# Kernel optimization log

Measured on AMD Instinct MI355X. Metric: run time of the kernel, lower is better.

The kernel has to match this reference:

```python
import jax, jax.numpy as jnp
import numpy as np

EMBED_DIM = 1024
NUM_HEADS = 16
HEAD_DIM = EMBED_DIM // NUM_HEADS
SCALING = HEAD_DIM ** -0.5
TGT_LEN, BSZ = 2048, 2


def setup_inputs() -> dict:
    key = jax.random.key(0)
    k1, k2, k3 = jax.random.split(key, 3)
    return {
        "query": jax.random.normal(k1, (TGT_LEN, BSZ, EMBED_DIM), jnp.float32),
        "in_proj_weight": jax.random.normal(k2, (3 * EMBED_DIM, EMBED_DIM), jnp.float32) * (EMBED_DIM ** -0.5),
        "in_proj_bias": jnp.zeros((3 * EMBED_DIM,), jnp.float32),
        "out_w": jax.random.normal(k3, (EMBED_DIM, EMBED_DIM), jnp.float32) * (EMBED_DIM ** -0.5),
        "out_b": jnp.zeros((EMBED_DIM,), jnp.float32),
    }


def reference(query, in_proj_weight, in_proj_bias, out_w, out_b):
    tgt_len, bsz, embed_dim = query.shape
    # fused QKV projection (self-attention path: qkv_same)
    qkv = query @ in_proj_weight.T + in_proj_bias  # [T, B, 3E]
    q, k, v = jnp.split(qkv, 3, axis=-1)
    q = q * SCALING
    # [T, B, E] -> [B*H, T, hd]
    def to_heads(x):
        return x.reshape(tgt_len, bsz * NUM_HEADS, HEAD_DIM).transpose(1, 0, 2)
    q, k, v = to_heads(q), to_heads(k), to_heads(v)
    attn_weights = jnp.einsum('bqd,bkd->bqk', q, k)          # [B*H, T, T]
    attn_weights = jax.nn.softmax(attn_weights, axis=-1)
    attn = jnp.einsum('bqk,bkd->bqd', attn_weights, v)       # [B*H, T, hd]
    attn = attn.transpose(1, 0, 2).reshape(tgt_len, bsz, embed_dim)
    attn = attn @ out_w.T + out_b
    # averaged attention weights over heads (need_weights=True)
    avg_weights = attn_weights.reshape(bsz, NUM_HEADS, tgt_len, tgt_len).mean(axis=1)
    return attn, avg_weights
```

## Files before the change

kernel.cpp:

```cpp
#include <hip/hip_runtime.h>
#include <hip/hip_bf16.h>
#include <math.h>

#define T_LEN 2048
#define BSZ   2
#define EMB   1024
#define NH    16
#define HD    64
#define BHN   (BSZ*NH)
#define M1    (T_LEN*BSZ)
#define SCAL  0.125f
#define QSCALE (0.125f * 1.44269504088896f)

typedef __attribute__((ext_vector_type(8))) short bf16x8;
typedef __attribute__((ext_vector_type(4))) float f32x4;
typedef __attribute__((ext_vector_type(2))) unsigned int u32x2;

__device__ inline unsigned short f2bf(float x) {
    union { float f; unsigned u; } v; v.f = x;
    unsigned r = v.u + 0x7FFF + ((v.u >> 16) & 1);
    return (unsigned short)(r >> 16);
}

__device__ inline unsigned pack2bf(float a, float b) {
    union { __hip_bfloat162 h; unsigned u; } v;
    v.h = __float22bfloat162_rn(make_float2(a, b));
    return v.u;
}

__device__ inline float fexp2(float x) {
#if __has_builtin(__builtin_amdgcn_exp2f)
    return __builtin_amdgcn_exp2f(x);
#else
    return exp2f(x);
#endif
}

__device__ inline void async16(const unsigned short* g, unsigned short* l) {
    __builtin_amdgcn_global_load_lds(
        (const __attribute__((address_space(1))) void*)g,
        (__attribute__((address_space(3))) void*)l, 16, 0, 0);
}

__device__ inline void hard_barrier() {
    __builtin_amdgcn_sched_barrier(0);
    asm volatile("" ::: "memory");
    __builtin_amdgcn_s_barrier();
    asm volatile("" ::: "memory");
    __builtin_amdgcn_sched_barrier(0);
}

__device__ inline unsigned short* swz(unsigned short* base, int r, int c) {
    return base + (((r << 3) + (c ^ (r & 7))) << 3);
}
__device__ inline const unsigned short* swz(const unsigned short* base, int r, int c) {
    return base + (((r << 3) + (c ^ (r & 7))) << 3);
}

__device__ inline void xchg(unsigned e, unsigned o, unsigned& w_lo, unsigned& w_hi) {
#if __has_builtin(__builtin_amdgcn_permlane32_swap) && __has_builtin(__builtin_amdgcn_permlane16_swap)
    u32x2 x = __builtin_amdgcn_permlane32_swap(e, o, false, false);
    u32x2 y = __builtin_amdgcn_permlane16_swap(x[0], x[1], false, false);
    w_lo = y[0]; w_hi = y[1];
#else
    int lane = (int)(threadIdx.x & 63);
    int quad = lane >> 4, l16 = lane & 15;
    int srcA = ((quad & 1) * 2) * 16 + l16;
    int srcB = ((quad & 1) * 2 + 1) * 16 + l16;
    unsigned ea = (unsigned)__shfl((int)e, srcA, 64);
    unsigned oa = (unsigned)__shfl((int)o, srcA, 64);
    unsigned eb = (unsigned)__shfl((int)e, srcB, 64);
    unsigned ob = (unsigned)__shfl((int)o, srcB, 64);
    w_lo = (quad >> 1) ? oa : ea;
    w_hi = (quad >> 1) ? ob : eb;
#endif
}

__global__ __launch_bounds__(256) void cvt3_kernel(
    const float* __restrict__ s0, const float* __restrict__ s1,
    const float* __restrict__ s2, unsigned short* __restrict__ dst,
    int n0, int n1)
{
    int idx = blockIdx.x * 256 + threadIdx.x;
    const float* src; int o;
    if (idx < n0)           { src = s0; o = idx; }
    else if (idx < n0 + n1) { src = s1; o = idx - n0; }
    else                    { src = s2; o = idx - n0 - n1; }
    float4 a = reinterpret_cast<const float4*>(src)[(size_t)o * 2];
    float4 c = reinterpret_cast<const float4*>(src)[(size_t)o * 2 + 1];
    unsigned w[4] = { pack2bf(a.x, a.y), pack2bf(a.z, a.w),
                      pack2bf(c.x, c.y), pack2bf(c.z, c.w) };
    reinterpret_cast<uint4*>(dst)[idx] = *reinterpret_cast<uint4*>(w);
}

__global__ __launch_bounds__(256) void qkv_mfma_kernel(
    const unsigned short* __restrict__ A, const unsigned short* __restrict__ B,
    const float* __restrict__ bias,
    unsigned short* __restrict__ Q16, unsigned short* __restrict__ K16,
    unsigned short* __restrict__ Vt16)
{
    constexpr int BM = 128, BN = 128, BK = 32, K = 1024;
    __shared__ unsigned short As[BM * BK];
    __shared__ unsigned short Bs[BN * BK];
    const int tid = threadIdx.x;
    const int lane = tid & 63, wave = tid >> 6;
    const int quad = lane >> 4, l16 = lane & 15;
    const int wr = wave >> 1, wc = wave & 1;
    const int m0 = blockIdx.x * BM, n0 = blockIdx.y * BN;

    f32x4 zero4 = {0.f, 0.f, 0.f, 0.f};
    f32x4 acc[4][4];
    #pragma unroll
    for (int i = 0; i < 4; ++i)
        #pragma unroll
        for (int j = 0; j < 4; ++j) acc[i][j] = zero4;

    for (int k0 = 0; k0 < K; k0 += BK) {
        __syncthreads();
        #pragma unroll
        for (int t = 0; t < 2; ++t) {
            int c = t * 256 + tid;
            int m = c >> 2, kb = c & 3;
            async16(&A[(size_t)(m0 + m) * K + k0 + kb * 8], &As[c * 8]);
            async16(&B[(size_t)(n0 + m) * K + k0 + kb * 8], &Bs[c * 8]);
        }
        __syncthreads();
        bf16x8 af[4], bfr[4];
        #pragma unroll
        for (int i = 0; i < 4; ++i) {
            af[i]  = *reinterpret_cast<const bf16x8*>(&As[(wr * 64 + i * 16 + l16) * BK + quad * 8]);
            bfr[i] = *reinterpret_cast<const bf16x8*>(&Bs[(wc * 64 + i * 16 + l16) * BK + quad * 8]);
        }
        #pragma unroll
        for (int i = 0; i < 4; ++i)
            #pragma unroll
            for (int j = 0; j < 4; ++j)
                acc[i][j] = __builtin_amdgcn_mfma_f32_16x16x32_bf16(af[i], bfr[j], acc[i][j], 0, 0, 0);
    }

    #pragma unroll
    for (int j = 0; j < 4; ++j) {
        int n = n0 + wc * 64 + j * 16 + l16;
        float bv = bias[n];
        int which = n >> 10;
        int c = n & 1023;
        int h = c >> 6, d = c & 63;
        #pragma unroll
        for (int i = 0; i < 4; ++i) {
            #pragma unroll
            for (int r = 0; r < 4; ++r) {
                int m = m0 + wr * 64 + i * 16 + quad * 4 + r;
                int t = m >> 1, b = m & 1;
                int bh = b * NH + h;
                float v = acc[i][j][r] + bv;
                if (which == 0)      Q16[((size_t)bh * T_LEN + t) * HD + d] = f2bf(v * QSCALE);
                else if (which == 1) K16[((size_t)bh * T_LEN + t) * HD + d] = f2bf(v);
                else                 Vt16[((size_t)bh * HD + d) * T_LEN + t] = f2bf(v);
            }
        }
    }
}

__global__ __launch_bounds__(256) void flash_mfma_kernel(
    const unsigned short* __restrict__ Qb, const unsigned short* __restrict__ Kb,
    const unsigned short* __restrict__ Vt, unsigned short* __restrict__ AO,
    float* __restrict__ Rrow)
{
    __shared__ unsigned short Ks[2][64 * 64];
    __shared__ unsigned short Vs[2][64 * 64];
    const int tid = threadIdx.x;
    const int lane = tid & 63, wave = tid >> 6;
    const int quad = lane >> 4, l16 = lane & 15;

    const int lin = blockIdx.y * gridDim.x + blockIdx.x;
    const int xcd = lin & 7, slot = lin >> 3;
    const int bh = xcd * 4 + (slot >> 5);
    const int qt = slot & 31;
    const int q0 = qt * 64;
    const int b = bh >> 4, h = bh & 15;

    const unsigned short* Qp = Qb + ((size_t)bh * T_LEN + q0 + wave * 16 + l16) * HD;
    bf16x8 qf0 = *reinterpret_cast<const bf16x8*>(Qp + quad * 8);
    bf16x8 qf1 = *reinterpret_cast<const bf16x8*>(Qp + 32 + quad * 8);

    f32x4 zero4 = {0.f, 0.f, 0.f, 0.f};
    f32x4 oacc[4] = {zero4, zero4, zero4, zero4};
    float l_i = 0.f;

    const unsigned short* Kbase = Kb + (size_t)bh * T_LEN * HD;
    const unsigned short* Vbase = Vt + (size_t)bh * HD * T_LEN;

    const int cl0 = tid, cl1 = tid + 256;
    const int r0 = cl0 >> 3, c0 = (cl0 & 7) ^ (r0 & 7);
    const int r1 = cl1 >> 3, c1 = (cl1 & 7) ^ (r1 & 7);

    async16(&Kbase[(size_t)r0 * HD + c0 * 8], &Ks[0][cl0 * 8]);
    async16(&Kbase[(size_t)r1 * HD + c1 * 8], &Ks[0][cl1 * 8]);
    async16(&Vbase[(size_t)r0 * T_LEN + c0 * 8], &Vs[0][cl0 * 8]);
    async16(&Vbase[(size_t)r1 * T_LEN + c1 * 8], &Vs[0][cl1 * 8]);

    int cur = 0;
    for (int kt = 0; kt < T_LEN; kt += 64) {
        if (kt + 64 < T_LEN) {
            const int nb = cur ^ 1, nkt = kt + 64;
            async16(&Kbase[(size_t)(nkt + r0) * HD + c0 * 8], &Ks[nb][cl0 * 8]);
            async16(&Kbase[(size_t)(nkt + r1) * HD + c1 * 8], &Ks[nb][cl1 * 8]);
            async16(&Vbase[(size_t)r0 * T_LEN + nkt + c0 * 8], &Vs[nb][cl0 * 8]);
            async16(&Vbase[(size_t)r1 * T_LEN + nkt + c1 * 8], &Vs[nb][cl1 * 8]);
            asm volatile("s_waitcnt vmcnt(4)" ::: "memory");
        } else {
            asm volatile("s_waitcnt vmcnt(0)" ::: "memory");
        }
        hard_barrier();

        const unsigned short* Kt = Ks[cur];
        const unsigned short* Vv = Vs[cur];

        f32x4 sacc[4] = {zero4, zero4, zero4, zero4};
        __builtin_amdgcn_s_setprio(1);
        #pragma unroll
        for (int kb = 0; kb < 4; ++kb) {
            bf16x8 kf0 = *reinterpret_cast<const bf16x8*>(swz(Kt, kb * 16 + l16, quad));
            sacc[kb] = __builtin_amdgcn_mfma_f32_16x16x32_bf16(kf0, qf0, sacc[kb], 0, 0, 0);
            bf16x8 kf1 = *reinterpret_cast<const bf16x8*>(swz(Kt, kb * 16 + l16, 4 + quad));
            sacc[kb] = __builtin_amdgcn_mfma_f32_16x16x32_bf16(kf1, qf1, sacc[kb], 0, 0, 0);
        }
        __builtin_amdgcn_s_setprio(0);

        float psum = 0.f;
        unsigned dlo[4], dhi[4];
        #pragma unroll
        for (int kb = 0; kb < 4; ++kb) {
            float p0 = fexp2(sacc[kb][0]);
            float p1 = fexp2(sacc[kb][1]);
            float p2 = fexp2(sacc[kb][2]);
            float p3 = fexp2(sacc[kb][3]);
            psum += (p0 + p1) + (p2 + p3);
            dlo[kb] = pack2bf(p0, p1);
            dhi[kb] = pack2bf(p2, p3);
        }
        psum += __shfl_xor(psum, 16);
        psum += __shfl_xor(psum, 32);
        l_i += psum;

        bf16x8 pfrag[2];
        #pragma unroll
        for (int s = 0; s < 2; ++s) {
            unsigned w0, w1, w2, w3;
            xchg(dlo[2 * s], dlo[2 * s + 1], w0, w2);
            xchg(dhi[2 * s], dhi[2 * s + 1], w1, w3);
            union { bf16x8 v; unsigned u[4]; } P;
            P.u[0] = w0; P.u[1] = w1; P.u[2] = w2; P.u[3] = w3;
            pfrag[s] = P.v;
        }

        __builtin_amdgcn_s_setprio(1);
        #pragma unroll
        for (int s = 0; s < 2; ++s) {
            #pragma unroll
            for (int dt = 0; dt < 4; ++dt) {
                bf16x8 va = *reinterpret_cast<const bf16x8*>(swz(Vv, dt * 16 + l16, s * 4 + quad));
                oacc[dt] = __builtin_amdgcn_mfma_f32_16x16x32_bf16(va, pfrag[s], oacc[dt], 0, 0, 0);
            }
        }
        __builtin_amdgcn_s_setprio(0);

        hard_barrier();
        cur ^= 1;
    }

    float rl = 1.0f / l_i;
    int q = q0 + wave * 16 + l16;
    size_t base = ((size_t)q * BSZ + b) * EMB + h * HD;
    #pragma unroll
    for (int dt = 0; dt < 4; ++dt) {
        unsigned o[2] = { pack2bf(oacc[dt][0] * rl, oacc[dt][1] * rl),
                          pack2bf(oacc[dt][2] * rl, oacc[dt][3] * rl) };
        *reinterpret_cast<uint2*>(&AO[base + dt * 16 + quad * 4]) = *reinterpret_cast<uint2*>(o);
    }
    if (quad == 0)
        Rrow[(size_t)bh * T_LEN + q] = rl;
}

__global__ __launch_bounds__(256) void avg_mfma_kernel(
    const unsigned short* __restrict__ Qb, const unsigned short* __restrict__ Kb,
    const float* __restrict__ Rrow, float* __restrict__ avg_out)
{
    __shared__ unsigned short Ks[2][2][64 * 64];
    const int tid = threadIdx.x;
    const int lane = tid & 63, wave = tid >> 6;
    const int quad = lane >> 4, l16 = lane & 15;
    const int kt = blockIdx.x, qt = blockIdx.y, b = blockIdx.z;
    const int q0 = qt * 128, k0 = kt * 64;

    auto stage_pair = [&](int buf, int h0) {
        const unsigned short* Kg = Kb + ((size_t)(b * NH + h0) * T_LEN + k0) * HD;
        #pragma unroll
        for (int t = 0; t < 4; ++t) {
            int c = t * 256 + tid;
            int hh = c >> 9, cl = c & 511;
            int r = cl >> 3, cc = (cl & 7) ^ (r & 7);
            async16(&Kg[(size_t)hh * T_LEN * HD + (size_t)r * HD + cc * 8],
                    &Ks[buf][0][0] + (size_t)c * 8);
        }
    };

    f32x4 zero4 = {0.f, 0.f, 0.f, 0.f};
    f32x4 acc[2][4];
    #pragma unroll
    for (int s = 0; s < 2; ++s)
        #pragma unroll
        for (int c = 0; c < 4; ++c) acc[s][c] = zero4;

    stage_pair(0, 0);
    int cur = 0;
    for (int g = 0; g < NH / 2; ++g) {
        if (g + 1 < NH / 2) {
            stage_pair(cur ^ 1, 2 * (g + 1));
            asm volatile("s_waitcnt vmcnt(4)" ::: "memory");
        } else {
            asm volatile("s_waitcnt vmcnt(0)" ::: "memory");
        }
        hard_barrier();

        #pragma unroll
        for (int hh = 0; hh < 2; ++hh) {
            const int bh = b * NH + 2 * g + hh;
            const unsigned short* Kt = Ks[cur][hh];
            bf16x8 kf[4][2];
            #pragma unroll
            for (int c = 0; c < 4; ++c) {
                kf[c][0] = *reinterpret_cast<const bf16x8*>(swz(Kt, c * 16 + l16, quad));
                kf[c][1] = *reinterpret_cast<const bf16x8*>(swz(Kt, c * 16 + l16, 4 + quad));
            }
            #pragma unroll
            for (int s = 0; s < 2; ++s) {
                const int qrow = q0 + s * 64 + wave * 16;
                const unsigned short* Qp = Qb + ((size_t)bh * T_LEN + qrow + l16) * HD;
                bf16x8 qf0 = *reinterpret_cast<const bf16x8*>(Qp + quad * 8);
                bf16x8 qf1 = *reinterpret_cast<const bf16x8*>(Qp + 32 + quad * 8);
                float4 rlv = *reinterpret_cast<const float4*>(
                    &Rrow[(size_t)bh * T_LEN + qrow + quad * 4]);

                f32x4 sacc[4] = {zero4, zero4, zero4, zero4};
                __builtin_amdgcn_s_setprio(1);
                #pragma unroll
                for (int c = 0; c < 4; ++c) {
                    sacc[c] = __builtin_amdgcn_mfma_f32_16x16x32_bf16(qf0, kf[c][0], sacc[c], 0, 0, 0);
                    sacc[c] = __builtin_amdgcn_mfma_f32_16x16x32_bf16(qf1, kf[c][1], sacc[c], 0, 0, 0);
                }
                __builtin_amdgcn_s_setprio(0);

                float rl4[4] = { rlv.x, rlv.y, rlv.z, rlv.w };
                #pragma unroll
                for (int c = 0; c < 4; ++c)
                    #pragma unroll
                    for (int r = 0; r < 4; ++r)
                        acc[s][c][r] += fexp2(sacc[c][r]) * rl4[r];
            }
        }
        hard_barrier();
        cur ^= 1;
    }

    #pragma unroll
    for (int s = 0; s < 2; ++s)
        #pragma unroll
        for (int r = 0; r < 4; ++r) {
            int q = q0 + s * 64 + wave * 16 + quad * 4 + r;
            size_t base = ((size_t)b * T_LEN + q) * T_LEN + k0;
            #pragma unroll
            for (int c = 0; c < 4; ++c)
                avg_out[base + c * 16 + l16] = acc[s][c][r] * (1.0f / 16.0f);
        }
}

__global__ __launch_bounds__(256) void out_mfma_kernel(
    const unsigned short* __restrict__ A, const unsigned short* __restrict__ B,
    const float* __restrict__ bias, float* __restrict__ out)
{
    constexpr int BM = 128, BN = 128, BK = 32, K = 1024;
    __shared__ unsigned short As[BM * BK];
    __shared__ unsigned short Bs[BN * BK];
    const int tid = threadIdx.x;
    const int lane = tid & 63, wave = tid >> 6;
    const int quad = lane >> 4, l16 = lane & 15;
    const int wr = wave >> 1, wc = wave & 1;
    const int m0 = blockIdx.x * BM, n0 = blockIdx.y * BN;

    f32x4 zero4 = {0.f, 0.f, 0.f, 0.f};
    f32x4 acc[4][4];
    #pragma unroll
    for (int i = 0; i < 4; ++i)
        #pragma unroll
        for (int j = 0; j < 4; ++j) acc[i][j] = zero4;

    for (int k0 = 0; k0 < K; k0 += BK) {
        __syncthreads();
        #pragma unroll
        for (int t = 0; t < 2; ++t) {
            int c = t * 256 + tid;
            int m = c >> 2, kb = c & 3;
            async16(&A[(size_t)(m0 + m) * K + k0 + kb * 8], &As[c * 8]);
            async16(&B[(size_t)(n0 + m) * K + k0 + kb * 8], &Bs[c * 8]);
        }
        __syncthreads();
        bf16x8 af[4], bfr[4];
        #pragma unroll
        for (int i = 0; i < 4; ++i) {
            af[i]  = *reinterpret_cast<const bf16x8*>(&As[(wr * 64 + i * 16 + l16) * BK + quad * 8]);
            bfr[i] = *reinterpret_cast<const bf16x8*>(&Bs[(wc * 64 + i * 16 + l16) * BK + quad * 8]);
        }
        #pragma unroll
        for (int i = 0; i < 4; ++i)
            #pragma unroll
            for (int j = 0; j < 4; ++j)
                acc[i][j] = __builtin_amdgcn_mfma_f32_16x16x32_bf16(af[i], bfr[j], acc[i][j], 0, 0, 0);
    }

    #pragma unroll
    for (int j = 0; j < 4; ++j) {
        int n = n0 + wc * 64 + j * 16 + l16;
        float bv = bias[n];
        #pragma unroll
        for (int i = 0; i < 4; ++i) {
            #pragma unroll
            for (int r = 0; r < 4; ++r) {
                int m = m0 + wr * 64 + i * 16 + quad * 4 + r;
                out[(size_t)m * 1024 + n] = acc[i][j][r] + bv;
            }
        }
    }
}

extern "C" void kernel_launch(void* const* d_in, const int* in_sizes, int n_in,
                              void* d_out, int out_size, void* d_ws, size_t ws_size,
                              hipStream_t stream)
{
    const float* query = (const float*)d_in[0];
    const float* wqkv  = (const float*)d_in[1];
    const float* bqkv  = (const float*)d_in[2];
    const float* wout  = (const float*)d_in[3];
    const float* bout  = (const float*)d_in[4];
    float* out = (float*)d_out;

    char* ws = (char*)d_ws;
    const size_t E_Q   = (size_t)M1 * EMB;
    const size_t E_W   = (size_t)3 * EMB * EMB;
    const size_t E_WO  = (size_t)EMB * EMB;
    const size_t E_QKV = (size_t)BHN * T_LEN * HD;

    unsigned short* queryb = (unsigned short*)ws;
    unsigned short* wqkvb  = queryb + E_Q;
    unsigned short* woutb  = wqkvb + E_W;
    unsigned short* Q16    = woutb + E_WO;
    unsigned short* K16    = Q16 + E_QKV;
    unsigned short* Vt16   = K16 + E_QKV;
    unsigned short* AO16   = Vt16 + E_QKV;
    float* Lr = (float*)(AO16 + E_Q);
    const size_t need = (E_Q + E_W + E_WO + 4 * E_QKV) * 2 + (size_t)BHN * T_LEN * 4;
    if (ws_size < need) return;

    cvt3_kernel<<<(int)((E_Q + E_W + E_WO) / 8 / 256), 256, 0, stream>>>(
        query, wqkv, wout, queryb, (int)(E_Q / 8), (int)(E_W / 8));

    qkv_mfma_kernel<<<dim3(M1 / 128, 3072 / 128), 256, 0, stream>>>(queryb, wqkvb, bqkv, Q16, K16, Vt16);
    flash_mfma_kernel<<<dim3(T_LEN / 64, BHN), 256, 0, stream>>>(Q16, K16, Vt16, AO16, Lr);
    avg_mfma_kernel<<<dim3(T_LEN / 64, T_LEN / 128, BSZ), 256, 0, stream>>>(Q16, K16, Lr, out + (size_t)M1 * EMB);
    out_mfma_kernel<<<dim3(M1 / 128, 1024 / 128), 256, 0, stream>>>(AO16, woutb, bout, out);
}
```

Measured before the change: 252.2 us.

## Double flash attention query tile per block and relax barrier scheduling fences

Each wave in the flash kernel now handles two 16-row query slices, so a block covers 128 queries. K fragments are loaded once and reused across both slices, and each V fragment feeds two MFMAs. This halves the K/V tile loads per query and the grid size (512 blocks instead of 1024). The sched_barrier fences around s_barrier are removed in both attention kernels so the compiler can schedule across barriers, and launch bounds request 2 blocks per EU. The costs are higher register pressure and fewer blocks to fill the GPU.

```diff
diff --git a/kernel.cpp b/kernel.cpp
--- a/kernel.cpp
+++ b/kernel.cpp
@@ -42,12 +42,10 @@
         (__attribute__((address_space(3))) void*)l, 16, 0, 0);
 }
 
-__device__ inline void hard_barrier() {
-    __builtin_amdgcn_sched_barrier(0);
+__device__ inline void bar() {
     asm volatile("" ::: "memory");
     __builtin_amdgcn_s_barrier();
     asm volatile("" ::: "memory");
-    __builtin_amdgcn_sched_barrier(0);
 }
 
 __device__ inline unsigned short* swz(unsigned short* base, int r, int c) {
@@ -161,7 +159,7 @@
     }
 }
 
-__global__ __launch_bounds__(256) void flash_mfma_kernel(
+__global__ __launch_bounds__(256, 2) void flash_mfma_kernel(
     const unsigned short* __restrict__ Qb, const unsigned short* __restrict__ Kb,
     const unsigned short* __restrict__ Vt, unsigned short* __restrict__ AO,
     float* __restrict__ Rrow)
@@ -174,18 +172,27 @@
 
     const int lin = blockIdx.y * gridDim.x + blockIdx.x;
     const int xcd = lin & 7, slot = lin >> 3;
-    const int bh = xcd * 4 + (slot >> 5);
-    const int qt = slot & 31;
-    const int q0 = qt * 64;
+    const int bh = xcd * 4 + (slot >> 4);
+    const int qt = slot & 15;
+    const int q0 = qt * 128;
     const int b = bh >> 4, h = bh & 15;
 
-    const unsigned short* Qp = Qb + ((size_t)bh * T_LEN + q0 + wave * 16 + l16) * HD;
-    bf16x8 qf0 = *reinterpret_cast<const bf16x8*>(Qp + quad * 8);
-    bf16x8 qf1 = *reinterpret_cast<const bf16x8*>(Qp + 32 + quad * 8);
+    bf16x8 qf[2][2];
+    #pragma unroll
+    for (int s = 0; s < 2; ++s) {
+        const unsigned short* Qp =
+            Qb + ((size_t)bh * T_LEN + q0 + wave * 32 + s * 16 + l16) * HD;
+        qf[s][0] = *reinterpret_cast<const bf16x8*>(Qp + quad * 8);
+        qf[s][1] = *reinterpret_cast<const bf16x8*>(Qp + 32 + quad * 8);
+    }
 
     f32x4 zero4 = {0.f, 0.f, 0.f, 0.f};
-    f32x4 oacc[4] = {zero4, zero4, zero4, zero4};
-    float l_i = 0.f;
+    f32x4 oacc[2][4];
+    #pragma unroll
+    for (int s = 0; s < 2; ++s)
+        #pragma unroll
+        for (int dt = 0; dt < 4; ++dt) oacc[s][dt] = zero4;
+    float l_i[2] = {0.f, 0.f};
 
     const unsigned short* Kbase = Kb + (size_t)bh * T_LEN * HD;
     const unsigned short* Vbase = Vt + (size_t)bh * HD * T_LEN;
@@ -211,75 +218,87 @@
         } else {
             asm volatile("s_waitcnt vmcnt(0)" ::: "memory");
         }
-        hard_barrier();
+        bar();
 
         const unsigned short* Kt = Ks[cur];
         const unsigned short* Vv = Vs[cur];
 
-        f32x4 sacc[4] = {zero4, zero4, zero4, zero4};
+        bf16x8 kf[4][2];
+        #pragma unroll
+        for (int kb = 0; kb < 4; ++kb) {
+            kf[kb][0] = *reinterpret_cast<const bf16x8*>(swz(Kt, kb * 16 + l16, quad));
+            kf[kb][1] = *reinterpret_cast<const bf16x8*>(swz(Kt, kb * 16 + l16, 4 + quad));
+        }
+
+        bf16x8 pfrag[2][2];
+        #pragma unroll
+        for (int s = 0; s < 2; ++s) {
+            f32x4 sacc[4] = {zero4, zero4, zero4, zero4};
+            __builtin_amdgcn_s_setprio(1);
+            #pragma unroll
+            for (int kb = 0; kb < 4; ++kb) {
+                sacc[kb] = __builtin_amdgcn_mfma_f32_16x16x32_bf16(kf[kb][0], qf[s][0], sacc[kb], 0, 0, 0);
+                sacc[kb] = __builtin_amdgcn_mfma_f32_16x16x32_bf16(kf[kb][1], qf[s][1], sacc[kb], 0, 0, 0);
+            }
+            __builtin_amdgcn_s_setprio(0);
+
+            float psum = 0.f;
+            unsigned dlo[4], dhi[4];
+            #pragma unroll
+            for (int kb = 0; kb < 4; ++kb) {
+                float p0 = fexp2(sacc[kb][0]);
+                float p1 = fexp2(sacc[kb][1]);
+                float p2 = fexp2(sacc[kb][2]);
+                float p3 = fexp2(sacc[kb][3]);
+                psum += (p0 + p1) + (p2 + p3);
+                dlo[kb] = pack2bf(p0, p1);
+                dhi[kb] = pack2bf(p2, p3);
+            }
+            psum += __shfl_xor(psum, 16);
+            psum += __shfl_xor(psum, 32);
+            l_i[s] += psum;
+
+            #pragma unroll
+            for (int s2 = 0; s2 < 2; ++s2) {
+                unsigned w0, w1, w2, w3;
+                xchg(dlo[2 * s2], dlo[2 * s2 + 1], w0, w2);
+                xchg(dhi[2 * s2], dhi[2 * s2 + 1], w1, w3);
+                union { bf16x8 v; unsigned u[4]; } P;
+                P.u[0] = w0; P.u[1] = w1; P.u[2] = w2; P.u[3] = w3;
+                pfrag[s][s2] = P.v;
+            }
+        }
+
         __builtin_amdgcn_s_setprio(1);
         #pragma unroll
-        for (int kb = 0; kb < 4; ++kb) {
-            bf16x8 kf0 = *reinterpret_cast<const bf16x8*>(swz(Kt, kb * 16 + l16, quad));
-            sacc[kb] = __builtin_amdgcn_mfma_f32_16x16x32_bf16(kf0, qf0, sacc[kb], 0, 0, 0);
-            bf16x8 kf1 = *reinterpret_cast<const bf16x8*>(swz(Kt, kb * 16 + l16, 4 + quad));
-            sacc[kb] = __builtin_amdgcn_mfma_f32_16x16x32_bf16(kf1, qf1, sacc[kb], 0, 0, 0);
+        for (int ks = 0; ks < 2; ++ks) {
+            #pragma unroll
+            for (int dt = 0; dt < 4; ++dt) {
+                bf16x8 va = *reinterpret_cast<const bf16x8*>(swz(Vv, dt * 16 + l16, ks * 4 + quad));
+                oacc[0][dt] = __builtin_amdgcn_mfma_f32_16x16x32_bf16(va, pfrag[0][ks], oacc[0][dt], 0, 0, 0);
+                oacc[1][dt] = __builtin_amdgcn_mfma_f32_16x16x32_bf16(va, pfrag[1][ks], oacc[1][dt], 0, 0, 0);
+            }
         }
         __builtin_amdgcn_s_setprio(0);
 
-        float psum = 0.f;
-        unsigned dlo[4], dhi[4];
-        #pragma unroll
-        for (int kb = 0; kb < 4; ++kb) {
-            float p0 = fexp2(sacc[kb][0]);
-            float p1 = fexp2(sacc[kb][1]);
-            float p2 = fexp2(sacc[kb][2]);
-            float p3 = fexp2(sacc[kb][3]);
-            psum += (p0 + p1) + (p2 + p3);
-            dlo[kb] = pack2bf(p0, p1);
-            dhi[kb] = pack2bf(p2, p3);
-        }
-        psum += __shfl_xor(psum, 16);
-        psum += __shfl_xor(psum, 32);
-        l_i += psum;
-
-        bf16x8 pfrag[2];
-        #pragma unroll
-        for (int s = 0; s < 2; ++s) {
-            unsigned w0, w1, w2, w3;
-            xchg(dlo[2 * s], dlo[2 * s + 1], w0, w2);
-            xchg(dhi[2 * s], dhi[2 * s + 1], w1, w3);
-            union { bf16x8 v; unsigned u[4]; } P;
-            P.u[0] = w0; P.u[1] = w1; P.u[2] = w2; P.u[3] = w3;
-            pfrag[s] = P.v;
-        }
-
-        __builtin_amdgcn_s_setprio(1);
-        #pragma unroll
-        for (int s = 0; s < 2; ++s) {
-            #pragma unroll
-            for (int dt = 0; dt < 4; ++dt) {
-                bf16x8 va = *reinterpret_cast<const bf16x8*>(swz(Vv, dt * 16 + l16, s * 4 + quad));
-                oacc[dt] = __builtin_amdgcn_mfma_f32_16x16x32_bf16(va, pfrag[s], oacc[dt], 0, 0, 0);
-            }
-        }
-        __builtin_amdgcn_s_setprio(0);
-
-        hard_barrier();
+        bar();
         cur ^= 1;
     }
 
-    float rl = 1.0f / l_i;
-    int q = q0 + wave * 16 + l16;
-    size_t base = ((size_t)q * BSZ + b) * EMB + h * HD;
-    #pragma unroll
-    for (int dt = 0; dt < 4; ++dt) {
-        unsigned o[2] = { pack2bf(oacc[dt][0] * rl, oacc[dt][1] * rl),
-                          pack2bf(oacc[dt][2] * rl, oacc[dt][3] * rl) };
-        *reinterpret_cast<uint2*>(&AO[base + dt * 16 + quad * 4]) = *reinterpret_cast<uint2*>(o);
-    }
-    if (quad == 0)
-        Rrow[(size_t)bh * T_LEN + q] = rl;
+    #pragma unroll
+    for (int s = 0; s < 2; ++s) {
+        float rl = 1.0f / l_i[s];
+        int q = q0 + wave * 32 + s * 16 + l16;
+        size_t base = ((size_t)q * BSZ + b) * EMB + h * HD;
+        #pragma unroll
+        for (int dt = 0; dt < 4; ++dt) {
+            unsigned o[2] = { pack2bf(oacc[s][dt][0] * rl, oacc[s][dt][1] * rl),
+                              pack2bf(oacc[s][dt][2] * rl, oacc[s][dt][3] * rl) };
+            *reinterpret_cast<uint2*>(&AO[base + dt * 16 + quad * 4]) = *reinterpret_cast<uint2*>(o);
+        }
+        if (quad == 0)
+            Rrow[(size_t)bh * T_LEN + q] = rl;
+    }
 }
 
 __global__ __launch_bounds__(256) void avg_mfma_kernel(
@@ -321,7 +340,7 @@
         } else {
             asm volatile("s_waitcnt vmcnt(0)" ::: "memory");
         }
-        hard_barrier();
+        bar();
 
         #pragma unroll
         for (int hh = 0; hh < 2; ++hh) {
@@ -359,7 +378,7 @@
                         acc[s][c][r] += fexp2(sacc[c][r]) * rl4[r];
             }
         }
-        hard_barrier();
+        bar();
         cur ^= 1;
     }
 
@@ -465,7 +484,7 @@
         query, wqkv, wout, queryb, (int)(E_Q / 8), (int)(E_W / 8));
 
     qkv_mfma_kernel<<<dim3(M1 / 128, 3072 / 128), 256, 0, stream>>>(queryb, wqkvb, bqkv, Q16, K16, Vt16);
-    flash_mfma_kernel<<<dim3(T_LEN / 64, BHN), 256, 0, stream>>>(Q16, K16, Vt16, AO16, Lr);
+    flash_mfma_kernel<<<dim3(T_LEN / 128, BHN), 256, 0, stream>>>(Q16, K16, Vt16, AO16, Lr);
     avg_mfma_kernel<<<dim3(T_LEN / 64, T_LEN / 128, BSZ), 256, 0, stream>>>(Q16, K16, Lr, out + (size_t)M1 * EMB);
     out_mfma_kernel<<<dim3(M1 / 128, 1024 / 128), 256, 0, stream>>>(AO16, woutb, bout, out);
 }
```

Measured after the change: 248.5 us. Within noise of the previous version (-1.5%).

## Use 128-query tiles with 512-thread flash blocks and defer row-sum reduction

Applied to the files above, without the earlier changes.

The flash attention kernel now processes 128 query rows per block with 8 waves (512 threads), so each K/V tile staged in shared memory serves twice as many queries. Each thread issues one async load per K and V tile instead of two. The per-iteration cross-lane shuffle reduction of the softmax denominator moves to after the loop. The sched_barrier fences around the workgroup barriers are dropped so the compiler can schedule across them. Together these aim to cut global K/V traffic and per-iteration overhead, at the cost of fewer, larger blocks (512 blocks) and looser instruction-ordering control.

```diff
diff --git a/kernel.cpp b/kernel.cpp
--- a/kernel.cpp
+++ b/kernel.cpp
@@ -42,12 +42,10 @@
         (__attribute__((address_space(3))) void*)l, 16, 0, 0);
 }
 
-__device__ inline void hard_barrier() {
-    __builtin_amdgcn_sched_barrier(0);
+__device__ inline void bar() {
     asm volatile("" ::: "memory");
     __builtin_amdgcn_s_barrier();
     asm volatile("" ::: "memory");
-    __builtin_amdgcn_sched_barrier(0);
 }
 
 __device__ inline unsigned short* swz(unsigned short* base, int r, int c) {
@@ -161,7 +159,7 @@
     }
 }
 
-__global__ __launch_bounds__(256) void flash_mfma_kernel(
+__global__ __launch_bounds__(512, 4) void flash_mfma_kernel(
     const unsigned short* __restrict__ Qb, const unsigned short* __restrict__ Kb,
     const unsigned short* __restrict__ Vt, unsigned short* __restrict__ AO,
     float* __restrict__ Rrow)
@@ -174,44 +172,39 @@
 
     const int lin = blockIdx.y * gridDim.x + blockIdx.x;
     const int xcd = lin & 7, slot = lin >> 3;
-    const int bh = xcd * 4 + (slot >> 5);
-    const int qt = slot & 31;
-    const int q0 = qt * 64;
+    const int bh = xcd * 4 + (slot >> 4);
+    const int qt = slot & 15;
+    const int q0 = qt * 128;
     const int b = bh >> 4, h = bh & 15;
 
-    const unsigned short* Qp = Qb + ((size_t)bh * T_LEN + q0 + wave * 16 + l16) * HD;
+    const unsigned short* Qp =
+        Qb + ((size_t)bh * T_LEN + q0 + wave * 16 + l16) * HD;
     bf16x8 qf0 = *reinterpret_cast<const bf16x8*>(Qp + quad * 8);
     bf16x8 qf1 = *reinterpret_cast<const bf16x8*>(Qp + 32 + quad * 8);
 
     f32x4 zero4 = {0.f, 0.f, 0.f, 0.f};
     f32x4 oacc[4] = {zero4, zero4, zero4, zero4};
-    float l_i = 0.f;
+    float l_part = 0.f;
 
     const unsigned short* Kbase = Kb + (size_t)bh * T_LEN * HD;
     const unsigned short* Vbase = Vt + (size_t)bh * HD * T_LEN;
 
-    const int cl0 = tid, cl1 = tid + 256;
-    const int r0 = cl0 >> 3, c0 = (cl0 & 7) ^ (r0 & 7);
-    const int r1 = cl1 >> 3, c1 = (cl1 & 7) ^ (r1 & 7);
-
-    async16(&Kbase[(size_t)r0 * HD + c0 * 8], &Ks[0][cl0 * 8]);
-    async16(&Kbase[(size_t)r1 * HD + c1 * 8], &Ks[0][cl1 * 8]);
-    async16(&Vbase[(size_t)r0 * T_LEN + c0 * 8], &Vs[0][cl0 * 8]);
-    async16(&Vbase[(size_t)r1 * T_LEN + c1 * 8], &Vs[0][cl1 * 8]);
+    const int r0 = tid >> 3, c0 = (tid & 7) ^ (r0 & 7);
+
+    async16(&Kbase[(size_t)r0 * HD + c0 * 8], &Ks[0][tid * 8]);
+    async16(&Vbase[(size_t)r0 * T_LEN + c0 * 8], &Vs[0][tid * 8]);
 
     int cur = 0;
     for (int kt = 0; kt < T_LEN; kt += 64) {
         if (kt + 64 < T_LEN) {
             const int nb = cur ^ 1, nkt = kt + 64;
-            async16(&Kbase[(size_t)(nkt + r0) * HD + c0 * 8], &Ks[nb][cl0 * 8]);
-            async16(&Kbase[(size_t)(nkt + r1) * HD + c1 * 8], &Ks[nb][cl1 * 8]);
-            async16(&Vbase[(size_t)r0 * T_LEN + nkt + c0 * 8], &Vs[nb][cl0 * 8]);
-            async16(&Vbase[(size_t)r1 * T_LEN + nkt + c1 * 8], &Vs[nb][cl1 * 8]);
-            asm volatile("s_waitcnt vmcnt(4)" ::: "memory");
+            async16(&Kbase[(size_t)(nkt + r0) * HD + c0 * 8], &Ks[nb][tid * 8]);
+            async16(&Vbase[(size_t)r0 * T_LEN + nkt + c0 * 8], &Vs[nb][tid * 8]);
+            asm volatile("s_waitcnt vmcnt(2)" ::: "memory");
         } else {
             asm volatile("s_waitcnt vmcnt(0)" ::: "memory");
         }
-        hard_barrier();
+        bar();
 
         const unsigned short* Kt = Ks[cur];
         const unsigned short* Vv = Vs[cur];
@@ -227,7 +220,6 @@
         }
         __builtin_amdgcn_s_setprio(0);
 
-        float psum = 0.f;
         unsigned dlo[4], dhi[4];
         #pragma unroll
         for (int kb = 0; kb < 4; ++kb) {
@@ -235,41 +227,40 @@
             float p1 = fexp2(sacc[kb][1]);
             float p2 = fexp2(sacc[kb][2]);
             float p3 = fexp2(sacc[kb][3]);
-            psum += (p0 + p1) + (p2 + p3);
+            l_part += (p0 + p1) + (p2 + p3);
             dlo[kb] = pack2bf(p0, p1);
             dhi[kb] = pack2bf(p2, p3);
         }
-        psum += __shfl_xor(psum, 16);
-        psum += __shfl_xor(psum, 32);
-        l_i += psum;
 
         bf16x8 pfrag[2];
         #pragma unroll
-        for (int s = 0; s < 2; ++s) {
+        for (int ks = 0; ks < 2; ++ks) {
             unsigned w0, w1, w2, w3;
-            xchg(dlo[2 * s], dlo[2 * s + 1], w0, w2);
-            xchg(dhi[2 * s], dhi[2 * s + 1], w1, w3);
+            xchg(dlo[2 * ks], dlo[2 * ks + 1], w0, w2);
+            xchg(dhi[2 * ks], dhi[2 * ks + 1], w1, w3);
             union { bf16x8 v; unsigned u[4]; } P;
             P.u[0] = w0; P.u[1] = w1; P.u[2] = w2; P.u[3] = w3;
-            pfrag[s] = P.v;
+            pfrag[ks] = P.v;
         }
 
         __builtin_amdgcn_s_setprio(1);
         #pragma unroll
-        for (int s = 0; s < 2; ++s) {
+        for (int ks = 0; ks < 2; ++ks) {
             #pragma unroll
             for (int dt = 0; dt < 4; ++dt) {
-                bf16x8 va = *reinterpret_cast<const bf16x8*>(swz(Vv, dt * 16 + l16, s * 4 + quad));
-                oacc[dt] = __builtin_amdgcn_mfma_f32_16x16x32_bf16(va, pfrag[s], oacc[dt], 0, 0, 0);
+                bf16x8 va = *reinterpret_cast<const bf16x8*>(swz(Vv, dt * 16 + l16, ks * 4 + quad));
+                oacc[dt] = __builtin_amdgcn_mfma_f32_16x16x32_bf16(va, pfrag[ks], oacc[dt], 0, 0, 0);
             }
         }
         __builtin_amdgcn_s_setprio(0);
 
-        hard_barrier();
+        bar();
         cur ^= 1;
     }
 
-    float rl = 1.0f / l_i;
+    l_part += __shfl_xor(l_part, 16);
+    l_part += __shfl_xor(l_part, 32);
+    float rl = 1.0f / l_part;
     int q = q0 + wave * 16 + l16;
     size_t base = ((size_t)q * BSZ + b) * EMB + h * HD;
     #pragma unroll
@@ -321,7 +312,7 @@
         } else {
             asm volatile("s_waitcnt vmcnt(0)" ::: "memory");
         }
-        hard_barrier();
+        bar();
 
         #pragma unroll
         for (int hh = 0; hh < 2; ++hh) {
@@ -359,7 +350,7 @@
                         acc[s][c][r] += fexp2(sacc[c][r]) * rl4[r];
             }
         }
-        hard_barrier();
+        bar();
         cur ^= 1;
     }
 
@@ -465,7 +456,7 @@
         query, wqkv, wout, queryb, (int)(E_Q / 8), (int)(E_W / 8));
 
     qkv_mfma_kernel<<<dim3(M1 / 128, 3072 / 128), 256, 0, stream>>>(queryb, wqkvb, bqkv, Q16, K16, Vt16);
-    flash_mfma_kernel<<<dim3(T_LEN / 64, BHN), 256, 0, stream>>>(Q16, K16, Vt16, AO16, Lr);
+    flash_mfma_kernel<<<dim3(T_LEN / 128, BHN), 512, 0, stream>>>(Q16, K16, Vt16, AO16, Lr);
     avg_mfma_kernel<<<dim3(T_LEN / 64, T_LEN / 128, BSZ), 256, 0, stream>>>(Q16, K16, Lr, out + (size_t)M1 * EMB);
     out_mfma_kernel<<<dim3(M1 / 128, 1024 / 128), 256, 0, stream>>>(AO16, woutb, bout, out);
 }
```

Measured after the change: 242.3 us. 1.04x faster.
